# Optimization experiments

Hardware: AMD Instinct MI355X
Metric: run time of the kernel (lower is better)

## Reference

```python
import jax, jax.numpy as jnp
import numpy as np

B, D, T = 4, 1024, 512      # z: [B, input_dim, T]
V, CD = 32000, 4096          # codebook: [codebook_size, codebook_dim]
EPS = 1e-12                  # F.normalize default eps


def setup_inputs() -> dict:
    key = jax.random.key(0)
    k1, k2, k3, k4 = jax.random.split(key, 4)
    z = jax.random.normal(k1, (B, D, T), dtype=jnp.float32)
    codebook = jax.random.normal(k2, (V, CD), dtype=jnp.float32) * 0.02
    cb_w = jax.random.normal(k3, (D, CD), dtype=jnp.float32) * 0.02  # torch Linear weight [out,in]
    cb_b = jax.random.normal(k4, (D,), dtype=jnp.float32) * 0.02
    return {"z": z, "codebook": codebook, "cb_w": cb_w, "cb_b": cb_b}


def _l2norm(x):
    n = jnp.sqrt(jnp.sum(x * x, axis=1, keepdims=True))
    return x / jnp.maximum(n, EPS)


def reference(z, codebook, cb_w, cb_b):
    # stride == 1, use_cblinear == True -> z_e = z
    z_e = z                                              # [B, D, T]
    proj_cb = codebook @ cb_w.T + cb_b                    # [V, D] cb_proj(codebook)

    # decode_latents
    enc = jnp.transpose(z_e, (0, 2, 1)).reshape(-1, D)    # (B*T, D)
    enc_n = _l2norm(enc)
    cb_n = _l2norm(proj_cb)
    dist = (jnp.sum(enc_n * enc_n, axis=1, keepdims=True)
            - 2.0 * enc_n @ cb_n.T
            + jnp.sum(cb_n * cb_n, axis=1)[None, :])      # (B*T, V)
    indices = jnp.argmax(-dist, axis=1).reshape(B, T)     # argmin distance
    z_q = jnp.transpose(proj_cb[indices], (0, 2, 1))      # gather un-normalized codes -> [B, D, T]

    commitment_loss = jnp.mean((z_e - jax.lax.stop_gradient(z_q)) ** 2, axis=(1, 2))  # [B]
    codebook_loss = jnp.mean((z_q - jax.lax.stop_gradient(z_e)) ** 2, axis=(1, 2))    # [B]
    z_q_st = z_e + jax.lax.stop_gradient(z_q - z_e)       # straight-through
    return z_q_st, indices, commitment_loss, codebook_loss
```

## Files before the change

### kernel.cpp

```cpp
#include <hip/hip_runtime.h>
#include <hip/hip_bf16.h>
#include <math.h>

#define B_  4
#define D_  1024
#define T_  512
#define V_  32000
#define CD_ 4096
#define NR  (B_*T_)
#define VT2 (V_/256)
#define NTILE1 ((V_/256)*(D_/256))

typedef __attribute__((ext_vector_type(8))) short short8v;
typedef __attribute__((ext_vector_type(4))) float f32x4;

#define MFMA16(a,b,c) __builtin_amdgcn_mfma_f32_16x16x32_bf16((a),(b),(c),0,0,0)

#define ASM_VMCNT8() asm volatile("s_waitcnt vmcnt(8)" ::: "memory")
#define ASM_VMCNT0() asm volatile("s_waitcnt vmcnt(0)" ::: "memory")
#define ASM_LGKM0()  asm volatile("s_waitcnt lgkmcnt(0)" ::: "memory")
#define SCHED_BAR()  __builtin_amdgcn_sched_barrier(0)

__device__ __forceinline__ unsigned short f2bf(float f) {
    return __builtin_bit_cast(unsigned short, __float2bfloat16(f));
}
__device__ __forceinline__ float bf2f(unsigned short u) {
    unsigned int v = ((unsigned int)u) << 16;
    return __builtin_bit_cast(float, v);
}
__device__ __forceinline__ void glds16(const unsigned short* g, unsigned short* l) {
    __builtin_amdgcn_global_load_lds(
        (const __attribute__((address_space(1))) unsigned int*)g,
        (__attribute__((address_space(3))) unsigned int*)l, 16, 0, 0);
}
__device__ __forceinline__ void cvt8(const float4& x, const float4& y,
                                     short8v& h, short8v& l) {
    float xs[8] = {x.x, x.y, x.z, x.w, y.x, y.y, y.z, y.w};
    #pragma unroll
    for (int e = 0; e < 8; ++e) {
        unsigned short hb = f2bf(xs[e]);
        h[e] = (short)hb;
        l[e] = (short)f2bf(xs[e] - bf2f(hb));
    }
}
__device__ __forceinline__ int xcd_swz(int wg, int nwg) {
    int q = nwg >> 3, r = nwg & 7;
    int x = wg & 7, o = wg >> 3;
    return (x < r ? x * (q + 1) : r * (q + 1) + (x - r) * q) + o;
}

__global__ __launch_bounds__(256) void vq_cvt8(const float* __restrict__ x,
                                               unsigned short* __restrict__ hi,
                                               unsigned short* __restrict__ lo,
                                               size_t n8) {
    size_t stride = (size_t)gridDim.x * 256;
    for (size_t i = (size_t)blockIdx.x * 256 + threadIdx.x; i < n8; i += stride) {
        float4 a = *(const float4*)(x + 8 * i);
        float4 b = *(const float4*)(x + 8 * i + 4);
        short8v h, l;
        cvt8(a, b, h, l);
        *(short8v*)(hi + 8 * i) = h;
        *(short8v*)(lo + 8 * i) = l;
    }
}

#define T8_PHASE(pp, EXTRA)                                                   \
    {                                                                         \
        short8v aAh = *(const short8v*)&smem[cur][0][(wr8 + 2*(pp)) * 512 + lane8];     \
        short8v aAl = *(const short8v*)&smem[cur][1][(wr8 + 2*(pp)) * 512 + lane8];     \
        short8v aBh = *(const short8v*)&smem[cur][0][(wr8 + 2*(pp) + 1) * 512 + lane8]; \
        short8v aBl = *(const short8v*)&smem[cur][1][(wr8 + 2*(pp) + 1) * 512 + lane8]; \
        EXTRA;                                                                \
        SCHED_BAR();                                                          \
        __builtin_amdgcn_s_barrier();                                         \
        ASM_LGKM0();                                                          \
        SCHED_BAR();                                                          \
        __builtin_amdgcn_s_setprio(1);                                        \
        _Pragma("unroll")                                                     \
        for (int nf = 0; nf < 4; ++nf) {                                      \
            acc[2*(pp)][nf]   = MFMA16(aAh, bh[nf], acc[2*(pp)][nf]);         \
            acc[2*(pp)][nf]   = MFMA16(aAh, bl[nf], acc[2*(pp)][nf]);         \
            acc[2*(pp)][nf]   = MFMA16(aAl, bh[nf], acc[2*(pp)][nf]);         \
            acc[2*(pp)+1][nf] = MFMA16(aBh, bh[nf], acc[2*(pp)+1][nf]);       \
            acc[2*(pp)+1][nf] = MFMA16(aBh, bl[nf], acc[2*(pp)+1][nf]);       \
            acc[2*(pp)+1][nf] = MFMA16(aBl, bh[nf], acc[2*(pp)+1][nf]);       \
        }                                                                     \
        __builtin_amdgcn_s_setprio(0);                                        \
        __builtin_amdgcn_s_barrier();                                         \
        SCHED_BAR();                                                          \
    }

__global__ __launch_bounds__(512, 2) void vq_gemm1_t8(
    const unsigned short* __restrict__ Ahp, const unsigned short* __restrict__ Alp,
    const unsigned short* __restrict__ Bhp, const unsigned short* __restrict__ Blp,
    const float* __restrict__ bias,
    unsigned short* __restrict__ Phi, unsigned short* __restrict__ Plo)
{
    __shared__ unsigned short smem[2][4][8192];
    const int wg = xcd_swz(blockIdx.x, NTILE1);
    const int mt = (wg >> 2) * 256;
    const int nt = (wg & 3) * 256;
    const int lane = threadIdx.x & 63, w = threadIdx.x >> 6;
    const int wr = w >> 2, wc = w & 3;
    const int r16 = lane & 15, kg = lane >> 4;
    const int lane8 = lane * 8, wr8 = wr * 8, wc4 = wc * 4;
    const int pw = w >> 1;
    const unsigned short* gplane = (pw == 0) ? Ahp : (pw == 1) ? Alp
                                   : (pw == 2) ? Bhp : Blp;
    const int baseRow = (pw < 2 ? mt : nt) + (w & 1) * 128 + r16;
    const unsigned short* gsrc = gplane + (size_t)baseRow * CD_ + kg * 8;
    unsigned short* lb0 = &smem[0][pw][(w & 1) * 4096 + lane8];
    unsigned short* lb1 = &smem[1][pw][(w & 1) * 4096 + lane8];

    f32x4 acc[8][4];
    #pragma unroll
    for (int i = 0; i < 8; ++i)
        #pragma unroll
        for (int j = 0; j < 4; ++j) acc[i][j] = (f32x4){0.f, 0.f, 0.f, 0.f};

    #pragma unroll
    for (int q = 0; q < 8; ++q)
        glds16(gsrc + (size_t)q * 16 * CD_, lb0 + q * 512);
    ASM_VMCNT0();
    __builtin_amdgcn_s_barrier();
    SCHED_BAR();
    const int NT = CD_ / 32;
    for (int t = 0; t < NT; ++t) {
        const int cur = t & 1;
        unsigned short* lbN = cur ? lb0 : lb1;
        short8v bh[4], bl[4];
        #pragma unroll
        for (int nf = 0; nf < 4; ++nf) {
            bh[nf] = *(const short8v*)&smem[cur][2][(wc4 + nf) * 512 + lane8];
            bl[nf] = *(const short8v*)&smem[cur][3][(wc4 + nf) * 512 + lane8];
        }
        T8_PHASE(0,
            if (t + 1 < NT) {
                const size_t kof = (size_t)(t + 1) * 32;
                _Pragma("unroll")
                for (int q = 0; q < 8; ++q)
                    glds16(gsrc + kof + (size_t)q * 16 * CD_, lbN + q * 512);
            })
        T8_PHASE(1, (void)0)
        T8_PHASE(2, (void)0)
        T8_PHASE(3, if (t + 1 < NT) { ASM_VMCNT0(); })
    }

    #pragma unroll
    for (int nf = 0; nf < 4; ++nf) {
        const int col = nt + wc * 64 + nf * 16 + r16;
        const float bv = bias[col];
        #pragma unroll
        for (int mf = 0; mf < 8; ++mf) {
            const int rbase = mt + wr * 128 + mf * 16 + kg * 4;
            #pragma unroll
            for (int r = 0; r < 4; ++r) {
                float vv = acc[mf][nf][r] + bv;
                unsigned short h = f2bf(vv);
                unsigned short l = f2bf(vv - bf2f(h));
                size_t o = (size_t)(rbase + r) * D_ + col;
                Phi[o] = h; Plo[o] = l;
            }
        }
    }
}

__global__ __launch_bounds__(512, 2) void vq_gemm2_t8(
    const unsigned short* __restrict__ Ahp, const unsigned short* __restrict__ Alp,
    const unsigned short* __restrict__ Bhp, const unsigned short* __restrict__ Blp,
    const float* __restrict__ ninv,
    float* __restrict__ pmax, int* __restrict__ pidx)
{
    __shared__ unsigned short smem[2][4][8192];
    const int wg = xcd_swz(blockIdx.x, (NR/256) * VT2);
    const int nid = wg >> 3;
    const int mt = (wg & 7) * 256;
    const int nt = nid * 256;

    f32x4 acc[8][4];
    #pragma unroll
    for (int i = 0; i < 8; ++i)
        #pragma unroll
        for (int j = 0; j < 4; ++j) acc[i][j] = (f32x4){0.f, 0.f, 0.f, 0.f};
    const int lane = threadIdx.x & 63, w = threadIdx.x >> 6;
    const int wr = w >> 2, wc = w & 3;
    const int r16 = lane & 15, kg = lane >> 4;
    const int lane8 = lane * 8, wr8 = wr * 8, wc4 = wc * 4;
    const int pw = w >> 1;
    const unsigned short* gplane = (pw == 0) ? Ahp : (pw == 1) ? Alp
                                   : (pw == 2) ? Bhp : Blp;
    const int baseRow = (pw < 2 ? mt : nt) + (w & 1) * 128 + r16;
    const unsigned short* gsrc = gplane + (size_t)baseRow * D_ + kg * 8;
    unsigned short* lb0 = &smem[0][pw][(w & 1) * 4096 + lane8];
    unsigned short* lb1 = &smem[1][pw][(w & 1) * 4096 + lane8];
    #pragma unroll
    for (int q = 0; q < 8; ++q)
        glds16(gsrc + (size_t)q * 16 * D_, lb0 + q * 512);
    ASM_VMCNT0();
    __builtin_amdgcn_s_barrier();
    SCHED_BAR();
    const int NT = D_ / 32;
    for (int t = 0; t < NT; ++t) {
        const int cur = t & 1;
        unsigned short* lbN = cur ? lb0 : lb1;
        short8v bh[4], bl[4];
        #pragma unroll
        for (int nf = 0; nf < 4; ++nf) {
            bh[nf] = *(const short8v*)&smem[cur][2][(wc4 + nf) * 512 + lane8];
            bl[nf] = *(const short8v*)&smem[cur][3][(wc4 + nf) * 512 + lane8];
        }
        T8_PHASE(0,
            if (t + 1 < NT) {
                const size_t kof = (size_t)(t + 1) * 32;
                _Pragma("unroll")
                for (int q = 0; q < 8; ++q)
                    glds16(gsrc + kof + (size_t)q * 16 * D_, lbN + q * 512);
            })
        T8_PHASE(1, (void)0)
        T8_PHASE(2, (void)0)
        T8_PHASE(3, if (t + 1 < NT) { ASM_VMCNT0(); })
    }

    float* redv = (float*)&smem[0][0][0];
    int*   redi = (int*)&smem[0][0][2048];
    float nv[4];
    #pragma unroll
    for (int nf = 0; nf < 4; ++nf) nv[nf] = ninv[nt + wc * 64 + nf * 16 + r16];
    #pragma unroll
    for (int mf = 0; mf < 8; ++mf) {
        #pragma unroll
        for (int r = 0; r < 4; ++r) {
            float best = -INFINITY; int bi = 0x7fffffff;
            #pragma unroll
            for (int nf = 0; nf < 4; ++nf) {
                float v = acc[mf][nf][r] * nv[nf];
                int ci = nt + wc * 64 + nf * 16 + r16;
                if (v > best || (v == best && ci < bi)) { best = v; bi = ci; }
            }
            #pragma unroll
            for (int m = 8; m >= 1; m >>= 1) {
                float ov = __shfl_xor(best, m, 16);
                int   oi = __shfl_xor(bi,   m, 16);
                if (ov > best || (ov == best && oi < bi)) { best = ov; bi = oi; }
            }
            if (r16 == 0) {
                int rl = wr * 128 + mf * 16 + kg * 4 + r;
                redv[rl * 4 + wc] = best; redi[rl * 4 + wc] = bi;
            }
        }
    }
    __builtin_amdgcn_s_barrier();
    if (threadIdx.x < 256) {
        float best = -INFINITY; int bi = 0x7fffffff;
        #pragma unroll
        for (int c = 0; c < 4; ++c) {
            float v = redv[threadIdx.x * 4 + c];
            int   i = redi[threadIdx.x * 4 + c];
            if (v > best || (v == best && i < bi)) { best = v; bi = i; }
        }
        size_t o = (size_t)(mt + threadIdx.x) * VT2 + nid;
        pmax[o] = best; pidx[o] = bi;
    }
}

__global__ __launch_bounds__(256) void vq_norms_pl(const unsigned short* __restrict__ ph,
                                                   const unsigned short* __restrict__ pl,
                                                   float* __restrict__ ninv) {
    const int row  = blockIdx.x * 4 + (threadIdx.x >> 6);
    const int lane = threadIdx.x & 63;
    float s = 0.f;
    #pragma unroll
    for (int q = 0; q < 2; ++q) {
        size_t o = (size_t)row * D_ + q * 512 + lane * 8;
        short8v h = *(const short8v*)(ph + o);
        short8v l = *(const short8v*)(pl + o);
        #pragma unroll
        for (int e = 0; e < 8; ++e) {
            float x = bf2f((unsigned short)h[e]) + bf2f((unsigned short)l[e]);
            s += x * x;
        }
    }
    #pragma unroll
    for (int off = 32; off >= 1; off >>= 1) s += __shfl_down(s, off);
    if (lane == 0) ninv[row] = 1.0f / fmaxf(sqrtf(s), 1e-12f);
}

__global__ __launch_bounds__(256) void vq_transpose_cvt(const float* __restrict__ z,
                                                        unsigned short* __restrict__ ehi,
                                                        unsigned short* __restrict__ elo) {
    __shared__ float tile[64][65];
    const int b = blockIdx.z, t0 = blockIdx.x * 64, d0 = blockIdx.y * 64;
    const int lane = threadIdx.x & 63, sub = threadIdx.x >> 6;
    for (int dd = sub; dd < 64; dd += 4)
        tile[dd][lane] = z[((size_t)b * D_ + d0 + dd) * T_ + t0 + lane];
    __syncthreads();
    for (int tt = sub; tt < 64; tt += 4) {
        float v = tile[lane][tt];
        unsigned short h = f2bf(v);
        unsigned short l = f2bf(v - bf2f(h));
        size_t o = (size_t)(b * T_ + t0 + tt) * D_ + d0 + lane;
        ehi[o] = h; elo[o] = l;
    }
}

__global__ __launch_bounds__(256) void vq_argmerge(const float* __restrict__ pmax,
                                                   const int* __restrict__ pidx,
                                                   int* __restrict__ idxw,
                                                   float* __restrict__ outI,
                                                   int vt) {
    const int i = blockIdx.x * 256 + threadIdx.x;
    if (i >= NR) return;
    float best = -INFINITY; int bi = 0;
    for (int c = 0; c < vt; c++) {
        float v = pmax[(size_t)i * vt + c];
        int   ii = pidx[(size_t)i * vt + c];
        if (v > best || (v == best && ii < bi)) { best = v; bi = ii; }
    }
    idxw[i] = bi;
    outI[i] = (float)bi;
}

__global__ __launch_bounds__(256) void vq_gather_pl(const unsigned short* __restrict__ ph,
                                                    const unsigned short* __restrict__ pl,
                                                    const int* __restrict__ idxw,
                                                    const float* __restrict__ z,
                                                    float* __restrict__ out0,
                                                    float* __restrict__ lpart) {
    __shared__ float zq[64][65];
    __shared__ int idx_s[64];
    __shared__ float wsum[4];
    const int b = blockIdx.z, t0 = blockIdx.x * 64, d0 = blockIdx.y * 64;
    const int tid = threadIdx.x;
    const int lane = tid & 63, sub = tid >> 6;
    if (tid < 64) idx_s[tid] = idxw[b * T_ + t0 + tid];
    __syncthreads();
    for (int tt = sub; tt < 64; tt += 4) {
        size_t o = (size_t)idx_s[tt] * D_ + d0 + lane;
        zq[tt][lane] = bf2f(ph[o]) + bf2f(pl[o]);
    }
    __syncthreads();
    float lacc = 0.f;
    for (int dd = sub; dd < 64; dd += 4) {
        const size_t base = ((size_t)b * D_ + d0 + dd) * T_ + t0 + lane;
        float q = zq[lane][dd];
        float zv = z[base];
        out0[base] = q;
        float dv = zv - q;
        lacc += dv * dv;
    }
    #pragma unroll
    for (int off = 32; off >= 1; off >>= 1) lacc += __shfl_down(lacc, off);
    if (lane == 0) wsum[sub] = lacc;
    __syncthreads();
    if (tid == 0)
        lpart[(blockIdx.z * 16 + blockIdx.y) * 8 + blockIdx.x] =
            wsum[0] + wsum[1] + wsum[2] + wsum[3];
}

__global__ void vq_loss(const float* __restrict__ lpart, float* __restrict__ outL) {
    const int b = threadIdx.x;
    if (b >= B_) return;
    float s = 0.f;
    for (int q = 0; q < 128; q++) s += lpart[b * 128 + q];
    s /= (float)(D_ * T_);
    outL[b]      = s;
    outL[B_ + b] = s;
}

extern "C" void kernel_launch(void* const* d_in, const int* in_sizes, int n_in,
                              void* d_out, int out_size, void* d_ws, size_t ws_size,
                              hipStream_t stream) {
    const float* z        = (const float*)d_in[0];
    const float* codebook = (const float*)d_in[1];
    const float* cb_w     = (const float*)d_in[2];
    const float* cb_b     = (const float*)d_in[3];

    float* out0 = (float*)d_out;
    float* outI = out0 + (size_t)B_*D_*T_;
    float* outL = outI + NR;

    char* p = (char*)d_ws;
    auto alloc = [&](size_t bytes) { char* r = p; p += (bytes + 255) & ~(size_t)255; return r; };
    unsigned short* w_hi = (unsigned short*)alloc((size_t)D_ * CD_ * 2);
    unsigned short* w_lo = (unsigned short*)alloc((size_t)D_ * CD_ * 2);
    unsigned short* p_hi = (unsigned short*)alloc((size_t)V_ * D_ * 2);
    unsigned short* p_lo = (unsigned short*)alloc((size_t)V_ * D_ * 2);
    unsigned short* e_hi = (unsigned short*)alloc((size_t)NR * D_ * 2);
    unsigned short* e_lo = (unsigned short*)alloc((size_t)NR * D_ * 2);
    float* ninv  = (float*)alloc((size_t)V_ * 4);
    float* pmax  = (float*)alloc((size_t)NR * VT2 * 4);
    int*   pidx  = (int*)  alloc((size_t)NR * VT2 * 4);
    int*   idxw  = (int*)  alloc((size_t)NR * 4);
    float* lpart = (float*)alloc((size_t)2048 * 4);
    unsigned short* c_hi = (unsigned short*)alloc((size_t)V_ * CD_ * 2);
    unsigned short* c_lo = (unsigned short*)alloc((size_t)V_ * CD_ * 2);

    vq_cvt8<<<512, 256, 0, stream>>>(cb_w, w_hi, w_lo, (size_t)D_ * CD_ / 8);
    vq_transpose_cvt<<<dim3(T_/64, D_/64, B_), 256, 0, stream>>>(z, e_hi, e_lo);
    vq_cvt8<<<2048, 256, 0, stream>>>(codebook, c_hi, c_lo, (size_t)V_ * CD_ / 8);

    vq_gemm1_t8<<<NTILE1, 512, 0, stream>>>(c_hi, c_lo, w_hi, w_lo,
                                            cb_b, p_hi, p_lo);
    vq_norms_pl<<<V_/4, 256, 0, stream>>>(p_hi, p_lo, ninv);
    vq_gemm2_t8<<<(NR/256) * VT2, 512, 0, stream>>>(e_hi, e_lo, p_hi, p_lo,
                                                    ninv, pmax, pidx);
    vq_argmerge<<<NR/256, 256, 0, stream>>>(pmax, pidx, idxw, outI, VT2);
    vq_gather_pl<<<dim3(T_/64, D_/64, B_), 256, 0, stream>>>(p_hi, p_lo, idxw, z,
                                                             out0, lpart);
    vq_loss<<<1, 64, 0, stream>>>(lpart, outL);
}
```

Baseline: 1.539 ms.

## Replace double-buffered projection GEMM with single-buffer higher-occupancy variant

Replaces the codebook projection GEMM kernel with a version that uses one shared-memory buffer instead of two, halving LDS use, and raises the launch-bounds occupancy hint from 2 to 4 blocks. The intent is to hide memory latency by running more concurrent workgroups instead of prefetching within a block. In exchange, global loads no longer overlap MFMA work inside a block. The tighter register budget may force accumulator spills, and LDS capacity may still cap residency.

```diff
diff --git a/kernel.cpp b/kernel.cpp
--- a/kernel.cpp
+++ b/kernel.cpp
@@ -61,6 +61,99 @@
         cvt8(a, b, h, l);
         *(short8v*)(hi + 8 * i) = h;
         *(short8v*)(lo + 8 * i) = l;
+    }
+}
+
+__global__ __launch_bounds__(512, 4) void vq_gemm1_sb(
+    const unsigned short* __restrict__ Ahp, const unsigned short* __restrict__ Alp,
+    const unsigned short* __restrict__ Bhp, const unsigned short* __restrict__ Blp,
+    const float* __restrict__ bias,
+    unsigned short* __restrict__ Phi, unsigned short* __restrict__ Plo)
+{
+    __shared__ unsigned short smem[4][8192];
+    const int wg = xcd_swz(blockIdx.x, NTILE1);
+    const int mt = (wg >> 2) * 256;
+    const int nt = (wg & 3) * 256;
+    const int lane = threadIdx.x & 63, w = threadIdx.x >> 6;
+    const int wr = w >> 2, wc = w & 3;
+    const int r16 = lane & 15, kg = lane >> 4;
+    const int lane8 = lane * 8, wr8 = wr * 8, wc4 = wc * 4;
+    const int pw = w >> 1;
+    const unsigned short* gplane = (pw == 0) ? Ahp : (pw == 1) ? Alp
+                                   : (pw == 2) ? Bhp : Blp;
+    const int baseRow = (pw < 2 ? mt : nt) + (w & 1) * 128 + r16;
+    const unsigned short* gsrc = gplane + (size_t)baseRow * CD_ + kg * 8;
+    unsigned short* lb = &smem[pw][(w & 1) * 4096 + lane8];
+
+    f32x4 acc[8][4];
+    #pragma unroll
+    for (int i = 0; i < 8; ++i)
+        #pragma unroll
+        for (int j = 0; j < 4; ++j) acc[i][j] = (f32x4){0.f, 0.f, 0.f, 0.f};
+
+    #pragma unroll
+    for (int q = 0; q < 8; ++q)
+        glds16(gsrc + (size_t)q * 16 * CD_, lb + q * 512);
+    ASM_VMCNT0();
+    __builtin_amdgcn_s_barrier();
+    SCHED_BAR();
+
+    const int NT = CD_ / 32;
+    for (int t = 0; t < NT; ++t) {
+        short8v bh[4], bl[4];
+        #pragma unroll
+        for (int nf = 0; nf < 4; ++nf) {
+            bh[nf] = *(const short8v*)&smem[2][(wc4 + nf) * 512 + lane8];
+            bl[nf] = *(const short8v*)&smem[3][(wc4 + nf) * 512 + lane8];
+        }
+        #pragma unroll
+        for (int g = 0; g < 4; ++g) {
+            short8v a0h = *(const short8v*)&smem[0][(wr8 + 2*g) * 512 + lane8];
+            short8v a0l = *(const short8v*)&smem[1][(wr8 + 2*g) * 512 + lane8];
+            short8v a1h = *(const short8v*)&smem[0][(wr8 + 2*g + 1) * 512 + lane8];
+            short8v a1l = *(const short8v*)&smem[1][(wr8 + 2*g + 1) * 512 + lane8];
+            __builtin_amdgcn_s_setprio(1);
+            #pragma unroll
+            for (int nf = 0; nf < 4; ++nf) {
+                acc[2*g][nf]   = MFMA16(a0h, bh[nf], acc[2*g][nf]);
+                acc[2*g][nf]   = MFMA16(a0h, bl[nf], acc[2*g][nf]);
+                acc[2*g][nf]   = MFMA16(a0l, bh[nf], acc[2*g][nf]);
+                acc[2*g+1][nf] = MFMA16(a1h, bh[nf], acc[2*g+1][nf]);
+                acc[2*g+1][nf] = MFMA16(a1h, bl[nf], acc[2*g+1][nf]);
+                acc[2*g+1][nf] = MFMA16(a1l, bh[nf], acc[2*g+1][nf]);
+            }
+            __builtin_amdgcn_s_setprio(0);
+        }
+        ASM_LGKM0();
+        __builtin_amdgcn_s_barrier();
+        SCHED_BAR();
+        if (t + 1 < NT) {
+            const size_t kof = (size_t)(t + 1) * 32;
+            #pragma unroll
+            for (int q = 0; q < 8; ++q)
+                glds16(gsrc + kof + (size_t)q * 16 * CD_, lb + q * 512);
+            ASM_VMCNT0();
+            __builtin_amdgcn_s_barrier();
+            SCHED_BAR();
+        }
+    }
+
+    #pragma unroll
+    for (int nf = 0; nf < 4; ++nf) {
+        const int col = nt + wc * 64 + nf * 16 + r16;
+        const float bv = bias[col];
+        #pragma unroll
+        for (int mf = 0; mf < 8; ++mf) {
+            const int rbase = mt + wr * 128 + mf * 16 + kg * 4;
+            #pragma unroll
+            for (int r = 0; r < 4; ++r) {
+                float vv = acc[mf][nf][r] + bv;
+                unsigned short h = f2bf(vv);
+                unsigned short l = f2bf(vv - bf2f(h));
+                size_t o = (size_t)(rbase + r) * D_ + col;
+                Phi[o] = h; Plo[o] = l;
+            }
+        }
     }
 }
 
@@ -90,81 +183,6 @@
         SCHED_BAR();                                                          \
     }
 
-__global__ __launch_bounds__(512, 2) void vq_gemm1_t8(
-    const unsigned short* __restrict__ Ahp, const unsigned short* __restrict__ Alp,
-    const unsigned short* __restrict__ Bhp, const unsigned short* __restrict__ Blp,
-    const float* __restrict__ bias,
-    unsigned short* __restrict__ Phi, unsigned short* __restrict__ Plo)
-{
-    __shared__ unsigned short smem[2][4][8192];
-    const int wg = xcd_swz(blockIdx.x, NTILE1);
-    const int mt = (wg >> 2) * 256;
-    const int nt = (wg & 3) * 256;
-    const int lane = threadIdx.x & 63, w = threadIdx.x >> 6;
-    const int wr = w >> 2, wc = w & 3;
-    const int r16 = lane & 15, kg = lane >> 4;
-    const int lane8 = lane * 8, wr8 = wr * 8, wc4 = wc * 4;
-    const int pw = w >> 1;
-    const unsigned short* gplane = (pw == 0) ? Ahp : (pw == 1) ? Alp
-                                   : (pw == 2) ? Bhp : Blp;
-    const int baseRow = (pw < 2 ? mt : nt) + (w & 1) * 128 + r16;
-    const unsigned short* gsrc = gplane + (size_t)baseRow * CD_ + kg * 8;
-    unsigned short* lb0 = &smem[0][pw][(w & 1) * 4096 + lane8];
-    unsigned short* lb1 = &smem[1][pw][(w & 1) * 4096 + lane8];
-
-    f32x4 acc[8][4];
-    #pragma unroll
-    for (int i = 0; i < 8; ++i)
-        #pragma unroll
-        for (int j = 0; j < 4; ++j) acc[i][j] = (f32x4){0.f, 0.f, 0.f, 0.f};
-
-    #pragma unroll
-    for (int q = 0; q < 8; ++q)
-        glds16(gsrc + (size_t)q * 16 * CD_, lb0 + q * 512);
-    ASM_VMCNT0();
-    __builtin_amdgcn_s_barrier();
-    SCHED_BAR();
-    const int NT = CD_ / 32;
-    for (int t = 0; t < NT; ++t) {
-        const int cur = t & 1;
-        unsigned short* lbN = cur ? lb0 : lb1;
-        short8v bh[4], bl[4];
-        #pragma unroll
-        for (int nf = 0; nf < 4; ++nf) {
-            bh[nf] = *(const short8v*)&smem[cur][2][(wc4 + nf) * 512 + lane8];
-            bl[nf] = *(const short8v*)&smem[cur][3][(wc4 + nf) * 512 + lane8];
-        }
-        T8_PHASE(0,
-            if (t + 1 < NT) {
-                const size_t kof = (size_t)(t + 1) * 32;
-                _Pragma("unroll")
-                for (int q = 0; q < 8; ++q)
-                    glds16(gsrc + kof + (size_t)q * 16 * CD_, lbN + q * 512);
-            })
-        T8_PHASE(1, (void)0)
-        T8_PHASE(2, (void)0)
-        T8_PHASE(3, if (t + 1 < NT) { ASM_VMCNT0(); })
-    }
-
-    #pragma unroll
-    for (int nf = 0; nf < 4; ++nf) {
-        const int col = nt + wc * 64 + nf * 16 + r16;
-        const float bv = bias[col];
-        #pragma unroll
-        for (int mf = 0; mf < 8; ++mf) {
-            const int rbase = mt + wr * 128 + mf * 16 + kg * 4;
-            #pragma unroll
-            for (int r = 0; r < 4; ++r) {
-                float vv = acc[mf][nf][r] + bv;
-                unsigned short h = f2bf(vv);
-                unsigned short l = f2bf(vv - bf2f(h));
-                size_t o = (size_t)(rbase + r) * D_ + col;
-                Phi[o] = h; Plo[o] = l;
-            }
-        }
-    }
-}
-
 __global__ __launch_bounds__(512, 2) void vq_gemm2_t8(
     const unsigned short* __restrict__ Ahp, const unsigned short* __restrict__ Alp,
     const unsigned short* __restrict__ Bhp, const unsigned short* __restrict__ Blp,
@@ -399,7 +417,7 @@
     vq_transpose_cvt<<<dim3(T_/64, D_/64, B_), 256, 0, stream>>>(z, e_hi, e_lo);
     vq_cvt8<<<2048, 256, 0, stream>>>(codebook, c_hi, c_lo, (size_t)V_ * CD_ / 8);
 
-    vq_gemm1_t8<<<NTILE1, 512, 0, stream>>>(c_hi, c_lo, w_hi, w_lo,
+    vq_gemm1_sb<<<NTILE1, 512, 0, stream>>>(c_hi, c_lo, w_hi, w_lo,
                                             cb_b, p_hi, p_lo);
     vq_norms_pl<<<V_/4, 256, 0, stream>>>(p_hi, p_lo, ninv);
     vq_gemm2_t8<<<(NR/256) * VT2, 512, 0, stream>>>(e_hi, e_lo, p_hi, p_lo,
```

After: 3.636 ms. 136% more time.
